# Optimization experiments

Measured on AMD Instinct MI355X. Metric: run time of the kernel, lower is better.

Reference implementation:

```python
import jax, jax.numpy as jnp
import numpy as np

WINDOW = 15  # window_size from init


def setup_inputs() -> dict:
    key = jax.random.key(0)
    ks = jax.random.split(key, 8)
    B, S, H, G = 16, 4096, 768, 16
    sequence_output = jax.random.normal(ks[0], (B, S, H), dtype=jnp.float32)
    pooled_output = jax.random.normal(ks[1], (B, H), dtype=jnp.float32)
    token_type_ids = jnp.zeros((B, S), dtype=jnp.int64)
    word_mask = jax.random.randint(ks[2], (B, S), 0, 2, dtype=jnp.int64)
    gap_ids = jax.random.randint(ks[3], (B, G), 0, S, dtype=jnp.int64)
    gap_W = 0.02 * jax.random.normal(ks[4], (3 * H,), dtype=jnp.float32)
    gap_b = jnp.zeros((), dtype=jnp.float32)
    cls_W = 0.02 * jax.random.normal(ks[5], (3 * H,), dtype=jnp.float32)
    cls_b = jnp.zeros((), dtype=jnp.float32)
    return {"sequence_output": sequence_output, "pooled_output": pooled_output,
            "token_type_ids": token_type_ids, "word_mask": word_mask,
            "gap_ids": gap_ids, "gap_W": gap_W, "gap_b": gap_b,
            "cls_W": cls_W, "cls_b": cls_b}


def reference(sequence_output, pooled_output, token_type_ids, word_mask,
              gap_ids, gap_W, gap_b, cls_W, cls_b):
    B, S, H = sequence_output.shape
    G = gap_ids.shape[1]
    w = WINDOW
    Wlen = 2 * w + 1

    # gap token embeddings: [B, G, H]
    gaps = jnp.take_along_axis(sequence_output, gap_ids[:, :, None], axis=1)

    base_mask = (token_type_ids == 0) & (word_mask != 0)  # [B, S]

    # Sliding window gather around each gap (equivalent to the original
    # full-sequence masked reduction, since masked entries are exactly 0).
    offsets = jnp.arange(-w, w + 1)  # [Wlen]
    raw_idx = gap_ids[:, :, None] + offsets  # [B, G, Wlen]
    valid = (raw_idx >= 0) & (raw_idx < S)
    idx = jnp.clip(raw_idx, 0, S - 1)
    flat = idx.reshape(B, G * Wlen)
    win_mask = valid & jnp.take_along_axis(base_mask, flat, axis=1).reshape(B, G, Wlen)
    win_vals = jnp.take_along_axis(sequence_output, flat[:, :, None], axis=1).reshape(B, G, Wlen, H)

    # original does max(window * mask): masked positions contribute 0,
    # and the sequence always has positions outside the window -> max with 0
    masked_max = jnp.where(win_mask[..., None], win_vals, -jnp.inf).max(axis=2)
    window_max_pool = jnp.maximum(masked_max, 0.0)  # [B, G, H]
    num_tokens = win_mask.sum(axis=2).astype(jnp.float32)[:, :, None]
    window_avg_pool = jnp.einsum('bgw,bgwh->bgh', win_mask.astype(jnp.float32), win_vals) / num_tokens

    # full-text pooling
    text_masked_max = jnp.where(base_mask[:, :, None], sequence_output, -jnp.inf).max(axis=1)
    text_max_pool = jnp.maximum(text_masked_max, 0.0)  # [B, H]
    text_num = base_mask.sum(axis=1).astype(jnp.float32)[:, None]
    text_avg_pool = jnp.einsum('bs,bsh->bh', base_mask.astype(jnp.float32), sequence_output) / text_num

    gap_features = jnp.concatenate([gaps, window_max_pool, window_avg_pool], axis=-1)  # [B, G, 3H]
    cls_features = jnp.concatenate([pooled_output, text_max_pool, text_avg_pool], axis=-1)  # [B, 3H]

    gap_scores = gap_features @ gap_W + gap_b  # [B, G]
    cls_scores = (cls_features @ cls_W + cls_b)[:, None]  # [B, 1]
    return jnp.concatenate([cls_scores, gap_scores], axis=1)  # [B, 1+G]
```

## Files before the change

kernel.cpp:

```cpp
#include <hip/hip_runtime.h>
#include <math.h>

#define NB 16
#define NS 4096
#define NH 768
#define NG 16
#define WRAD 15
#define WLEN 31
#define NH4 192
#define OUTW (1 + NG)

__device__ inline float4 f4max(float4 a, float4 b) {
    return make_float4(fmaxf(a.x, b.x), fmaxf(a.y, b.y), fmaxf(a.z, b.z), fmaxf(a.w, b.w));
}
__device__ inline float4 f4add(float4 a, float4 b) {
    return make_float4(a.x + b.x, a.y + b.y, a.z + b.z, a.w + b.w);
}
__device__ inline float f4dot(float4 a, float4 b) {
    return a.x * b.x + a.y * b.y + a.z * b.z + a.w * b.w;
}

__device__ inline float block_reduce_192(float v, float* sbuf) {
    int tid = threadIdx.x;
    sbuf[tid] = v;
    if (tid < 64) sbuf[192 + tid] = 0.0f;
    __syncthreads();
    for (int off = 128; off > 0; off >>= 1) {
        if (tid < off) sbuf[tid] += sbuf[tid + off];
        __syncthreads();
    }
    float r = sbuf[0];
    __syncthreads();
    return r;
}

__global__ __launch_bounds__(192) void text_partial_kernel(
    const float* __restrict__ seq, const int* __restrict__ tt,
    const int* __restrict__ wm, float* __restrict__ pmax,
    float* __restrict__ psum, int chunk, int nchunks) {
    const int ss = blockIdx.x;
    const int b = blockIdx.y;
    const int tid = threadIdx.x;
    const int s0 = ss * chunk;

    __shared__ unsigned char valid[1024];
    for (int i = tid; i < chunk; i += blockDim.x) {
        const int s = s0 + i;
        valid[i] = (tt[b * NS + s] == 0) && (wm[b * NS + s] != 0);
    }
    __syncthreads();

    const float4* rowbase = (const float4*)(seq + (size_t)b * NS * NH);
    float4 mx = make_float4(-INFINITY, -INFINITY, -INFINITY, -INFINITY);
    float4 sm = make_float4(0.f, 0.f, 0.f, 0.f);
    for (int i = 0; i < chunk; ++i) {
        if (valid[i]) {
            float4 v = rowbase[(size_t)(s0 + i) * NH4 + tid];
            mx = f4max(mx, v);
            sm = f4add(sm, v);
        }
    }
    const size_t o = ((size_t)(b * nchunks + ss)) * NH4 + tid;
    ((float4*)pmax)[o] = mx;
    ((float4*)psum)[o] = sm;
}

__global__ __launch_bounds__(192) void cls_kernel(
    const float* __restrict__ pooled, const int* __restrict__ tt,
    const int* __restrict__ wm, const float* __restrict__ pmax,
    const float* __restrict__ psum, const float* __restrict__ clsW,
    const float* __restrict__ clsb, float* __restrict__ out, int nchunks) {
    const int b = blockIdx.x;
    const int tid = threadIdx.x;
    __shared__ float sbuf[256];

    float cnt = 0.f;
    for (int s = tid; s < NS; s += blockDim.x)
        cnt += (float)((tt[b * NS + s] == 0) && (wm[b * NS + s] != 0));
    const float count = block_reduce_192(cnt, sbuf);

    const float4* pm4 = (const float4*)pmax;
    const float4* ps4 = (const float4*)psum;
    float4 mx = make_float4(-INFINITY, -INFINITY, -INFINITY, -INFINITY);
    float4 sm = make_float4(0.f, 0.f, 0.f, 0.f);
    for (int c = 0; c < nchunks; ++c) {
        const size_t o = ((size_t)(b * nchunks + c)) * NH4 + tid;
        mx = f4max(mx, pm4[o]);
        sm = f4add(sm, ps4[o]);
    }
    const float4 zero4 = make_float4(0.f, 0.f, 0.f, 0.f);
    float4 tmax = f4max(mx, zero4);
    float4 tavg = make_float4(sm.x / count, sm.y / count, sm.z / count, sm.w / count);

    const float4* p4 = (const float4*)(pooled + (size_t)b * NH);
    const float4* w0 = (const float4*)clsW;
    const float4* w1 = (const float4*)(clsW + NH);
    const float4* w2 = (const float4*)(clsW + 2 * NH);
    float part = f4dot(p4[tid], w0[tid]) + f4dot(tmax, w1[tid]) + f4dot(tavg, w2[tid]);
    float total = block_reduce_192(part, sbuf);
    if (tid == 0) out[b * OUTW + 0] = total + clsb[0];
}

__global__ __launch_bounds__(192) void gap_kernel(
    const float* __restrict__ seq, const int* __restrict__ tt,
    const int* __restrict__ wm, const int* __restrict__ gids,
    const float* __restrict__ gapW, const float* __restrict__ gapb,
    float* __restrict__ out) {
    const int bg = blockIdx.x;
    const int b = bg / NG;
    const int g = bg % NG;
    const int tid = threadIdx.x;

    __shared__ int s_gid;
    __shared__ int s_valid[WLEN];
    __shared__ float s_cnt;
    __shared__ float sbuf[256];

    if (tid == 0) s_gid = gids[b * NG + g];
    __syncthreads();
    const int gi = s_gid;
    if (tid < WLEN) {
        const int idx = gi - WRAD + tid;
        s_valid[tid] = (idx >= 0 && idx < NS && tt[b * NS + idx] == 0 &&
                        wm[b * NS + idx] != 0) ? 1 : 0;
    }
    __syncthreads();
    if (tid == 0) {
        int c = 0;
        for (int j = 0; j < WLEN; ++j) c += s_valid[j];
        s_cnt = (float)c;
    }
    __syncthreads();
    const float count = s_cnt;

    const float4* rowbase = (const float4*)(seq + (size_t)b * NS * NH);
    const float4 gv = rowbase[(size_t)gi * NH4 + tid];

    float4 mx = make_float4(-INFINITY, -INFINITY, -INFINITY, -INFINITY);
    float4 sm = make_float4(0.f, 0.f, 0.f, 0.f);
    for (int j = 0; j < WLEN; ++j) {
        if (s_valid[j]) {
            float4 v = rowbase[(size_t)(gi - WRAD + j) * NH4 + tid];
            mx = f4max(mx, v);
            sm = f4add(sm, v);
        }
    }
    const float4 zero4 = make_float4(0.f, 0.f, 0.f, 0.f);
    float4 wmax = f4max(mx, zero4);
    float4 wavg = make_float4(sm.x / count, sm.y / count, sm.z / count, sm.w / count);

    const float4* w0 = (const float4*)gapW;
    const float4* w1 = (const float4*)(gapW + NH);
    const float4* w2 = (const float4*)(gapW + 2 * NH);
    float part = f4dot(gv, w0[tid]) + f4dot(wmax, w1[tid]) + f4dot(wavg, w2[tid]);
    float total = block_reduce_192(part, sbuf);
    if (tid == 0) out[b * OUTW + 1 + g] = total + gapb[0];
}

extern "C" void kernel_launch(void* const* d_in, const int* in_sizes, int n_in,
                              void* d_out, int out_size, void* d_ws, size_t ws_size,
                              hipStream_t stream) {
    const float* seq    = (const float*)d_in[0];
    const float* pooled = (const float*)d_in[1];
    const int*   tt     = (const int*)d_in[2];
    const int*   wm     = (const int*)d_in[3];
    const int*   gids   = (const int*)d_in[4];
    const float* gapW   = (const float*)d_in[5];
    const float* gapb   = (const float*)d_in[6];
    const float* clsW   = (const float*)d_in[7];
    const float* clsb   = (const float*)d_in[8];
    float* out = (float*)d_out;

    int nchunks = 64;
    while (nchunks > 4 &&
           (size_t)nchunks * NB * NH * 2 * sizeof(float) > ws_size)
        nchunks >>= 1;
    const int chunk = NS / nchunks;

    float* pmax = (float*)d_ws;
    float* psum = pmax + (size_t)nchunks * NB * NH;

    text_partial_kernel<<<dim3(nchunks, NB), 192, 0, stream>>>(
        seq, tt, wm, pmax, psum, chunk, nchunks);
    gap_kernel<<<NB * NG, 192, 0, stream>>>(seq, tt, wm, gids, gapW, gapb, out);
    cls_kernel<<<NB, 192, 0, stream>>>(pooled, tt, wm, pmax, psum, clsW, clsb,
                                       out, nchunks);
}
```

Baseline: 314.9 us.

## Fuse text-partial and gap kernels, compact valid rows, carry counts forward

Merges the text partial-reduction and gap-window kernels into one launch, where the first block range handles text chunks and the remaining blocks handle gaps. Text blocks build a compacted index list of valid rows with ballot/popcount and then load four rows at a time, so only valid rows are issued and more memory requests are in flight. Per-chunk valid counts are written out so the cls kernel no longer rescans the masks. The gap path loads all window rows without branching and selects values by predicate. The chunk count is now fixed at 32 and no longer checked against the workspace size.

Result: faster. 286.7 us (-8.9%).

```diff
diff --git a/kernel.cpp b/kernel.cpp
--- a/kernel.cpp
+++ b/kernel.cpp
@@ -9,6 +9,8 @@
 #define WLEN 31
 #define NH4 192
 #define OUTW (1 + NG)
+#define NCH 32
+#define CHUNK 128
 
 __device__ inline float4 f4max(float4 a, float4 b) {
     return make_float4(fmaxf(a.x, b.x), fmaxf(a.y, b.y), fmaxf(a.z, b.z), fmaxf(a.w, b.w));
@@ -34,63 +36,153 @@
     return r;
 }
 
-__global__ __launch_bounds__(192) void text_partial_kernel(
+__global__ __launch_bounds__(192) void fused_kernel(
     const float* __restrict__ seq, const int* __restrict__ tt,
-    const int* __restrict__ wm, float* __restrict__ pmax,
-    float* __restrict__ psum, int chunk, int nchunks) {
-    const int ss = blockIdx.x;
-    const int b = blockIdx.y;
+    const int* __restrict__ wm, const int* __restrict__ gids,
+    const float* __restrict__ gapW, const float* __restrict__ gapb,
+    float* __restrict__ pmax, float* __restrict__ psum,
+    int* __restrict__ pcnt, float* __restrict__ out) {
+    const int blk = blockIdx.x;
     const int tid = threadIdx.x;
-    const int s0 = ss * chunk;
-
-    __shared__ unsigned char valid[1024];
-    for (int i = tid; i < chunk; i += blockDim.x) {
-        const int s = s0 + i;
-        valid[i] = (tt[b * NS + s] == 0) && (wm[b * NS + s] != 0);
-    }
-    __syncthreads();
-
-    const float4* rowbase = (const float4*)(seq + (size_t)b * NS * NH);
-    float4 mx = make_float4(-INFINITY, -INFINITY, -INFINITY, -INFINITY);
-    float4 sm = make_float4(0.f, 0.f, 0.f, 0.f);
-    for (int i = 0; i < chunk; ++i) {
-        if (valid[i]) {
-            float4 v = rowbase[(size_t)(s0 + i) * NH4 + tid];
+
+    __shared__ float sbuf[256];
+    __shared__ int s_idx[CHUNK];
+    __shared__ unsigned long long s_wmask[2];
+    __shared__ int s_misc[2];
+
+    const float4 ninf4 = make_float4(-INFINITY, -INFINITY, -INFINITY, -INFINITY);
+    const float4 zero4 = make_float4(0.f, 0.f, 0.f, 0.f);
+
+    if (blk < NB * NCH) {
+        const int b = blk / NCH;
+        const int ss = blk % NCH;
+        const int s0 = ss * CHUNK;
+
+        if (tid < CHUNK) {
+            const int s = s0 + tid;
+            bool v = (tt[b * NS + s] == 0) && (wm[b * NS + s] != 0);
+            unsigned long long m = __ballot(v);
+            if ((tid & 63) == 0) s_wmask[tid >> 6] = m;
+        }
+        __syncthreads();
+        if (tid < CHUNK) {
+            const int w = tid >> 6, l = tid & 63;
+            const unsigned long long m = s_wmask[w];
+            if ((m >> l) & 1ull) {
+                int pos = (w ? __popcll(s_wmask[0]) : 0) +
+                          __popcll(m & ((1ull << l) - 1ull));
+                s_idx[pos] = s0 + tid;
+            }
+        }
+        if (tid == 0)
+            s_misc[0] = __popcll(s_wmask[0]) + __popcll(s_wmask[1]);
+        __syncthreads();
+        const int n = s_misc[0];
+
+        const float4* rowbase = (const float4*)(seq + (size_t)b * NS * NH);
+        float4 mx = ninf4;
+        float4 sm = zero4;
+        int i = 0;
+        for (; i + 4 <= n; i += 4) {
+            const int i0 = s_idx[i], i1 = s_idx[i + 1], i2 = s_idx[i + 2], i3 = s_idx[i + 3];
+            float4 v0 = rowbase[(size_t)i0 * NH4 + tid];
+            float4 v1 = rowbase[(size_t)i1 * NH4 + tid];
+            float4 v2 = rowbase[(size_t)i2 * NH4 + tid];
+            float4 v3 = rowbase[(size_t)i3 * NH4 + tid];
+            mx = f4max(mx, f4max(f4max(v0, v1), f4max(v2, v3)));
+            sm = f4add(sm, f4add(f4add(v0, v1), f4add(v2, v3)));
+        }
+        for (; i < n; ++i) {
+            float4 v = rowbase[(size_t)s_idx[i] * NH4 + tid];
             mx = f4max(mx, v);
             sm = f4add(sm, v);
         }
+        const size_t o = ((size_t)(b * NCH + ss)) * NH4 + tid;
+        ((float4*)pmax)[o] = mx;
+        ((float4*)psum)[o] = sm;
+        if (tid == 0) pcnt[b * NCH + ss] = n;
+    } else {
+        const int bg = blk - NB * NCH;
+        const int b = bg >> 4;
+        const int g = bg & 15;
+
+        if (tid == 0) s_misc[1] = gids[b * NG + g];
+        __syncthreads();
+        const int gi = s_misc[1];
+
+        if (tid < 64) {
+            bool v = false;
+            if (tid < WLEN) {
+                const int idx = gi - WRAD + tid;
+                v = (idx >= 0) && (idx < NS) && (tt[b * NS + idx] == 0) &&
+                    (wm[b * NS + idx] != 0);
+            }
+            unsigned long long m = __ballot(v);
+            if (tid == 0) s_wmask[0] = m;
+        }
+        __syncthreads();
+        const unsigned long long vm = s_wmask[0];
+        const float count = (float)__popcll(vm);
+
+        const float4* rowbase = (const float4*)(seq + (size_t)b * NS * NH);
+        const float4 gv = rowbase[(size_t)gi * NH4 + tid];
+
+        float4 mx = ninf4;
+        float4 sm = zero4;
+#pragma unroll 4
+        for (int j = 0; j < WLEN; ++j) {
+            int idx = gi - WRAD + j;
+            idx = idx < 0 ? 0 : (idx > NS - 1 ? NS - 1 : idx);
+            const float4 v = rowbase[(size_t)idx * NH4 + tid];
+            const bool val = (vm >> j) & 1ull;
+            mx.x = val ? fmaxf(mx.x, v.x) : mx.x;
+            mx.y = val ? fmaxf(mx.y, v.y) : mx.y;
+            mx.z = val ? fmaxf(mx.z, v.z) : mx.z;
+            mx.w = val ? fmaxf(mx.w, v.w) : mx.w;
+            sm.x += val ? v.x : 0.f;
+            sm.y += val ? v.y : 0.f;
+            sm.z += val ? v.z : 0.f;
+            sm.w += val ? v.w : 0.f;
+        }
+        const float4 wmax = f4max(mx, zero4);
+        const float4 wavg = make_float4(sm.x / count, sm.y / count,
+                                        sm.z / count, sm.w / count);
+
+        const float4* w0 = (const float4*)gapW;
+        const float4* w1 = (const float4*)(gapW + NH);
+        const float4* w2 = (const float4*)(gapW + 2 * NH);
+        float part = f4dot(gv, w0[tid]) + f4dot(wmax, w1[tid]) + f4dot(wavg, w2[tid]);
+        float total = block_reduce_192(part, sbuf);
+        if (tid == 0) out[b * OUTW + 1 + g] = total + gapb[0];
     }
-    const size_t o = ((size_t)(b * nchunks + ss)) * NH4 + tid;
-    ((float4*)pmax)[o] = mx;
-    ((float4*)psum)[o] = sm;
 }
 
 __global__ __launch_bounds__(192) void cls_kernel(
-    const float* __restrict__ pooled, const int* __restrict__ tt,
-    const int* __restrict__ wm, const float* __restrict__ pmax,
-    const float* __restrict__ psum, const float* __restrict__ clsW,
-    const float* __restrict__ clsb, float* __restrict__ out, int nchunks) {
+    const float* __restrict__ pooled, const float* __restrict__ pmax,
+    const float* __restrict__ psum, const int* __restrict__ pcnt,
+    const float* __restrict__ clsW, const float* __restrict__ clsb,
+    float* __restrict__ out) {
     const int b = blockIdx.x;
     const int tid = threadIdx.x;
     __shared__ float sbuf[256];
 
-    float cnt = 0.f;
-    for (int s = tid; s < NS; s += blockDim.x)
-        cnt += (float)((tt[b * NS + s] == 0) && (wm[b * NS + s] != 0));
-    const float count = block_reduce_192(cnt, sbuf);
+    float c = (tid < NCH) ? (float)pcnt[b * NCH + tid] : 0.f;
+    const float count = block_reduce_192(c, sbuf);
 
     const float4* pm4 = (const float4*)pmax;
     const float4* ps4 = (const float4*)psum;
     float4 mx = make_float4(-INFINITY, -INFINITY, -INFINITY, -INFINITY);
     float4 sm = make_float4(0.f, 0.f, 0.f, 0.f);
-    for (int c = 0; c < nchunks; ++c) {
-        const size_t o = ((size_t)(b * nchunks + c)) * NH4 + tid;
+#pragma unroll 8
+    for (int ch = 0; ch < NCH; ++ch) {
+        const size_t o = ((size_t)(b * NCH + ch)) * NH4 + tid;
         mx = f4max(mx, pm4[o]);
         sm = f4add(sm, ps4[o]);
     }
     const float4 zero4 = make_float4(0.f, 0.f, 0.f, 0.f);
-    float4 tmax = f4max(mx, zero4);
-    float4 tavg = make_float4(sm.x / count, sm.y / count, sm.z / count, sm.w / count);
+    const float4 tmax = f4max(mx, zero4);
+    const float4 tavg = make_float4(sm.x / count, sm.y / count,
+                                    sm.z / count, sm.w / count);
 
     const float4* p4 = (const float4*)(pooled + (size_t)b * NH);
     const float4* w0 = (const float4*)clsW;
@@ -99,62 +191,6 @@
     float part = f4dot(p4[tid], w0[tid]) + f4dot(tmax, w1[tid]) + f4dot(tavg, w2[tid]);
     float total = block_reduce_192(part, sbuf);
     if (tid == 0) out[b * OUTW + 0] = total + clsb[0];
-}
-
-__global__ __launch_bounds__(192) void gap_kernel(
-    const float* __restrict__ seq, const int* __restrict__ tt,
-    const int* __restrict__ wm, const int* __restrict__ gids,
-    const float* __restrict__ gapW, const float* __restrict__ gapb,
-    float* __restrict__ out) {
-    const int bg = blockIdx.x;
-    const int b = bg / NG;
-    const int g = bg % NG;
-    const int tid = threadIdx.x;
-
-    __shared__ int s_gid;
-    __shared__ int s_valid[WLEN];
-    __shared__ float s_cnt;
-    __shared__ float sbuf[256];
-
-    if (tid == 0) s_gid = gids[b * NG + g];
-    __syncthreads();
-    const int gi = s_gid;
-    if (tid < WLEN) {
-        const int idx = gi - WRAD + tid;
-        s_valid[tid] = (idx >= 0 && idx < NS && tt[b * NS + idx] == 0 &&
-                        wm[b * NS + idx] != 0) ? 1 : 0;
-    }
-    __syncthreads();
-    if (tid == 0) {
-        int c = 0;
-        for (int j = 0; j < WLEN; ++j) c += s_valid[j];
-        s_cnt = (float)c;
-    }
-    __syncthreads();
-    const float count = s_cnt;
-
-    const float4* rowbase = (const float4*)(seq + (size_t)b * NS * NH);
-    const float4 gv = rowbase[(size_t)gi * NH4 + tid];
-
-    float4 mx = make_float4(-INFINITY, -INFINITY, -INFINITY, -INFINITY);
-    float4 sm = make_float4(0.f, 0.f, 0.f, 0.f);
-    for (int j = 0; j < WLEN; ++j) {
-        if (s_valid[j]) {
-            float4 v = rowbase[(size_t)(gi - WRAD + j) * NH4 + tid];
-            mx = f4max(mx, v);
-            sm = f4add(sm, v);
-        }
-    }
-    const float4 zero4 = make_float4(0.f, 0.f, 0.f, 0.f);
-    float4 wmax = f4max(mx, zero4);
-    float4 wavg = make_float4(sm.x / count, sm.y / count, sm.z / count, sm.w / count);
-
-    const float4* w0 = (const float4*)gapW;
-    const float4* w1 = (const float4*)(gapW + NH);
-    const float4* w2 = (const float4*)(gapW + 2 * NH);
-    float part = f4dot(gv, w0[tid]) + f4dot(wmax, w1[tid]) + f4dot(wavg, w2[tid]);
-    float total = block_reduce_192(part, sbuf);
-    if (tid == 0) out[b * OUTW + 1 + g] = total + gapb[0];
 }
 
 extern "C" void kernel_launch(void* const* d_in, const int* in_sizes, int n_in,
@@ -171,18 +207,11 @@
     const float* clsb   = (const float*)d_in[8];
     float* out = (float*)d_out;
 
-    int nchunks = 64;
-    while (nchunks > 4 &&
-           (size_t)nchunks * NB * NH * 2 * sizeof(float) > ws_size)
-        nchunks >>= 1;
-    const int chunk = NS / nchunks;
-
     float* pmax = (float*)d_ws;
-    float* psum = pmax + (size_t)nchunks * NB * NH;
-
-    text_partial_kernel<<<dim3(nchunks, NB), 192, 0, stream>>>(
-        seq, tt, wm, pmax, psum, chunk, nchunks);
-    gap_kernel<<<NB * NG, 192, 0, stream>>>(seq, tt, wm, gids, gapW, gapb, out);
-    cls_kernel<<<NB, 192, 0, stream>>>(pooled, tt, wm, pmax, psum, clsW, clsb,
-                                       out, nchunks);
-}
+    float* psum = pmax + (size_t)NB * NCH * NH;
+    int*   pcnt = (int*)(psum + (size_t)NB * NCH * NH);
+
+    fused_kernel<<<NB * NCH + NB * NG, 192, 0, stream>>>(
+        seq, tt, wm, gids, gapW, gapb, pmax, psum, pcnt, out);
+    cls_kernel<<<NB, 192, 0, stream>>>(pooled, pmax, psum, pcnt, clsW, clsb, out);
+}
```
